# Kernel tuning notes

Hardware: AMD Instinct MI355X
Metric: run time of the kernel (lower is better)

## Reference

```python
import jax, jax.numpy as jnp
import numpy as np

K = 20

def lrelu(x):
    return jnp.where(x >= 0, x, 0.2 * x)

def get_graph_feature(x, k):
    # x: (B, N, C) channel-last. Returns (B, N, k, 2C) = [neighbor - x, x].
    inner = jnp.einsum('bnc,bmc->bnm', x, x)          # (B, N, N)
    sq = jnp.sum(x * x, axis=-1)                       # (B, N)
    # negative squared distance; top-k gives nearest neighbors (incl. self)
    neg_dist = 2.0 * inner - sq[:, :, None] - sq[:, None, :]
    _, idx = jax.lax.top_k(neg_dist, k)                # (B, N, k)
    neigh = jnp.take_along_axis(x[:, None, :, :], idx[:, :, :, None], axis=2)  # (B, N, k, C)
    center = jnp.broadcast_to(x[:, :, None, :], neigh.shape)
    return jnp.concatenate([neigh - center, center], axis=-1)

def setup_inputs() -> dict:
    key = jax.random.key(0)
    ks = jax.random.split(key, 12)
    B, N, input_dim = 32, 2048, 6
    emb_dim, out_dim = 1024, 40
    def w(k_, shape):
        fan_in = shape[-1]
        return jax.random.normal(k_, shape, dtype=jnp.float32) * (1.0 / np.sqrt(fan_in))
    return {
        'x':  jax.random.normal(ks[0], (B, N, input_dim), dtype=jnp.float32),
        'W1': w(ks[1], (64, 6)),            # conv1: 1x1 conv, no bias
        'W2': w(ks[2], (64, 128)),          # conv2
        'W5': w(ks[3], (emb_dim, 128)),     # conv5 (1d)
        'W3': w(ks[4], (32, input_dim - 3)),# conv3
        'W4': w(ks[5], (64, 32)),           # conv4
        'L1': w(ks[6], (128, (emb_dim + 64) * 2)),  # linear1, no bias
        'L2w': w(ks[7], (64, 128)),
        'L2b': jnp.zeros((64,), dtype=jnp.float32),
        'L3w': w(ks[8], (out_dim, 64)),
        'L3b': jnp.zeros((out_dim,), dtype=jnp.float32),
    }

def reference(x, W1, W2, W5, W3, W4, L1, L2w, L2b, L3w, L3b):
    x_pos = x[:, :, :3]       # (B, N, 3)
    x_feat = x[:, :, 3:]      # (B, N, input_dim-3)

    # EdgeConv block 1
    e = get_graph_feature(x_pos, K)                       # (B, N, k, 6)
    e = lrelu(jnp.einsum('bnkc,oc->bnko', e, W1))         # (B, N, k, 64)
    x1 = jnp.max(e, axis=2)                               # (B, N, 64)

    # EdgeConv block 2
    e = get_graph_feature(x1, K)                          # (B, N, k, 128)
    e = lrelu(jnp.einsum('bnkc,oc->bnko', e, W2))         # (B, N, k, 64)
    x2 = jnp.max(e, axis=2)                               # (B, N, 64)

    # conv5 over concatenated features
    h = jnp.concatenate([x1, x2], axis=-1)                # (B, N, 128)
    h = lrelu(jnp.einsum('bnc,oc->bno', h, W5))           # (B, N, emb)
    g = jnp.concatenate([jnp.max(h, axis=1), jnp.mean(h, axis=1)], axis=-1)  # (B, 2*emb)

    # per-point feature MLP (conv3 -> conv4)
    f = lrelu(jnp.einsum('bnc,oc->bno', x_feat, W3))      # (B, N, 32)
    f = lrelu(jnp.einsum('bnc,oc->bno', f, W4))           # (B, N, 64)
    fg = jnp.concatenate([jnp.max(f, axis=1), jnp.mean(f, axis=1)], axis=-1)  # (B, 128)

    z = jnp.concatenate([g, fg], axis=-1)                 # (B, (emb+64)*2)
    z = lrelu(z @ L1.T)
    z = lrelu(z @ L2w.T + L2b)
    return z @ L3w.T + L3b                                # (B, output)
```

## Files before the change

### kernel.cpp

```cpp
#include <hip/hip_runtime.h>
#include <math.h>

#define B_ 32
#define N_ 2048
#define KNN 20
#define FINF 3.402823466e38f
#define SCAP 256

typedef __attribute__((ext_vector_type(8))) short short8;
typedef __attribute__((ext_vector_type(4))) float f32x4;

#define OFF_X1   ((size_t)0)
#define OFF_X2   (OFF_X1 + (size_t)B_*N_*64*4)
#define OFF_SQ1  (OFF_X2 + (size_t)B_*N_*64*4)
#define OFF_IDX1 (OFF_SQ1 + (size_t)B_*N_*4)
#define OFF_IDX2 (OFF_IDX1 + (size_t)B_*N_*KNN*4)
#define OFF_PMAX (OFF_IDX2 + (size_t)B_*N_*KNN*4)
#define OFF_PSUM (OFF_PMAX + (size_t)B_*16*1024*4)
#define OFF_G    (OFF_PSUM + (size_t)B_*16*1024*4)
#define OFF_FG   (OFF_G + (size_t)B_*2048*4)
#define OFF_DIST (OFF_FG + (size_t)B_*128*4)
#define OFF_P    OFF_DIST
#define OFF_Q    (OFF_P + (size_t)B_*N_*64*4)
#define OFF_XHI  OFF_P
#define OFF_XLO  OFF_Q
#define OFF_WHI  (OFF_Q + (size_t)B_*N_*64*4)
#define OFF_WLO  (OFF_WHI + (size_t)1024*128*2)

__device__ __forceinline__ float lrelu(float x) { return x >= 0.0f ? x : 0.2f * x; }

template<class F>
__device__ __forceinline__ void wave_top20_slow(const float (&v)[32], int lane, int* out20, F idxf) {
    unsigned alive = 0xffffffffu;
    for (int sel = 0; sel < 20; ++sel) {
        float bv = -FINF;
        int bm = 0x7fffffff;
#pragma unroll
        for (int j = 0; j < 32; ++j) {
            bool a = (alive >> j) & 1u;
            bool better = a && (v[j] > bv);
            bv = better ? v[j] : bv;
            bm = better ? idxf(j) : bm;
        }
#pragma unroll
        for (int off = 32; off; off >>= 1) {
            float ov = __shfl_xor(bv, off, 64);
            int   om = __shfl_xor(bm, off, 64);
            bool take = (ov > bv) || (ov == bv && om < bm);
            bv = take ? ov : bv;
            bm = take ? om : bm;
        }
        if (lane == 0) out20[sel] = bm;
#pragma unroll
        for (int j = 0; j < 32; ++j)
            if (idxf(j) == bm) alive &= ~(1u << j);
    }
}

template<class F>
__device__ __forceinline__ void wave_top20_fast(const float (&v)[32], int lane,
                                                float* sval, int* sidx, int* out20, F idxf) {
    float lm = v[0];
#pragma unroll
    for (int j = 1; j < 32; ++j) lm = fmaxf(lm, v[j]);
    float s = lm;
#pragma unroll
    for (int k = 2; k <= 64; k <<= 1) {
#pragma unroll
        for (int j2 = k >> 1; j2 > 0; j2 >>= 1) {
            float o = __shfl_xor(s, j2, 64);
            bool up = ((lane & k) == 0);
            bool high = ((lane & j2) != 0);
            s = (high == up) ? fmaxf(s, o) : fminf(s, o);
        }
    }
    float that = __shfl(s, 44, 64);
    int cnt = 0;
    unsigned long long below = (lane == 63) ? 0xffffffffffffffffull >> 1
                                            : ((1ull << lane) - 1ull);
#pragma unroll
    for (int j = 0; j < 32; ++j) {
        bool p = (v[j] >= that);
        unsigned long long mk = __ballot(p);
        if (p) {
            int slot = cnt + (int)__popcll(mk & below);
            if (slot < SCAP) { sval[slot] = v[j]; sidx[slot] = idxf(j); }
        }
        cnt += (int)__popcll(mk);
    }
    int S = cnt;
    if (S > SCAP) {
        wave_top20_slow(v, lane, out20, idxf);
        return;
    }
    if (S <= 64) {
        bool ok = lane < S;
        float cv = ok ? sval[lane] : -FINF;
        int   cm = ok ? sidx[lane] : 0x7fffffff;
#pragma unroll
        for (int k = 2; k <= 64; k <<= 1) {
#pragma unroll
            for (int j2 = k >> 1; j2 > 0; j2 >>= 1) {
                float ov = __shfl_xor(cv, j2, 64);
                int   om = __shfl_xor(cm, j2, 64);
                bool up = ((lane & k) == 0);
                bool high = ((lane & j2) != 0);
                bool cur_first = (cv > ov) || (cv == ov && cm < om);
                bool take = (high == up) ? cur_first : !cur_first;
                cv = take ? ov : cv;
                cm = take ? om : cm;
            }
        }
        if (lane < 20) out20[lane] = cm;
    } else {
        float cv[4]; int cm[4]; unsigned alive = 0;
#pragma unroll
        for (int r = 0; r < 4; ++r) {
            int i = r * 64 + lane;
            bool ok = i < S;
            float vv = sval[i];
            int   mm = sidx[i];
            cv[r] = ok ? vv : -FINF;
            cm[r] = ok ? mm : 0x7fffffff;
            if (ok) alive |= 1u << r;
        }
        for (int sel = 0; sel < 20; ++sel) {
            float bv = -FINF; int bm = 0x7fffffff;
#pragma unroll
            for (int r = 0; r < 4; ++r) {
                bool a = (alive >> r) & 1u;
                bool better = a && (cv[r] > bv || (cv[r] == bv && cm[r] < bm));
                bv = better ? cv[r] : bv;
                bm = better ? cm[r] : bm;
            }
#pragma unroll
            for (int off = 32; off; off >>= 1) {
                float ov = __shfl_xor(bv, off, 64);
                int   om = __shfl_xor(bm, off, 64);
                bool take = (ov > bv) || (ov == bv && om < bm);
                bv = take ? ov : bv;
                bm = take ? om : bm;
            }
            if (lane == 0) out20[sel] = bm;
#pragma unroll
            for (int r = 0; r < 4; ++r)
                if (cm[r] == bm) alive &= ~(1u << r);
        }
    }
}

__global__ __launch_bounds__(256) void k1_knn_pos(const float* __restrict__ x,
                                                  int* __restrict__ idx1) {
    __shared__ float sP[N_ * 3];
    __shared__ float sval[4][SCAP];
    __shared__ int   sidx[4][SCAP];
    __shared__ int   sOut[4][20];
    int tid = threadIdx.x;
    int wid = tid >> 6, lane = tid & 63;
    int row = blockIdx.x * 4 + wid;
    int b = row >> 11, n = row & 2047;
    const float* xb = x + (size_t)b * N_ * 6;
    for (int m = tid; m < N_; m += 256) {
        float4 f = *(const float4*)(xb + m * 6);
        sP[m*3+0] = f.x; sP[m*3+1] = f.y; sP[m*3+2] = f.z;
    }
    __syncthreads();
    float cx = sP[n*3+0], cy = sP[n*3+1], cz = sP[n*3+2];
    float sqn = cx*cx + cy*cy + cz*cz;
    float v[32];
#pragma unroll
    for (int j = 0; j < 32; ++j) {
        int m = lane + (j << 6);
        float mx_ = sP[m*3+0], my = sP[m*3+1], mz = sP[m*3+2];
        float inner = cx*mx_ + cy*my + cz*mz;
        float sqm = mx_*mx_ + my*my + mz*mz;
        v[j] = 2.0f*inner - sqn - sqm;
    }
    wave_top20_fast(v, lane, sval[wid], sidx[wid], sOut[wid],
                    [lane](int j) { return lane + (j << 6); });
    __syncthreads();
    if (lane < 20) idx1[(size_t)row*KNN + lane] = sOut[wid][lane];
}

__global__ __launch_bounds__(256) void k2_conv1(const float* __restrict__ x,
                                                const int* __restrict__ idx1,
                                                const float* __restrict__ W1,
                                                float* __restrict__ x1,
                                                float* __restrict__ sq1) {
    int wid = threadIdx.x >> 6, o = threadIdx.x & 63;
    int row = blockIdx.x * 4 + wid;
    int b = row >> 11, n = row & 2047;
    const float* xb = x + (size_t)b * N_ * 6;
    float w0 = W1[o*6+0], w1 = W1[o*6+1], w2 = W1[o*6+2];
    float w3 = W1[o*6+3], w4 = W1[o*6+4], w5 = W1[o*6+5];
    float cx = xb[n*6+0], cy = xb[n*6+1], cz = xb[n*6+2];
    float base = w3*cx + w4*cy + w5*cz;
    float mx = -FINF;
    for (int k = 0; k < KNN; ++k) {
        int m = idx1[(size_t)row*KNN + k];
        float dx = xb[m*6+0]-cx, dy = xb[m*6+1]-cy, dz = xb[m*6+2]-cz;
        float s = base + w0*dx + w1*dy + w2*dz;
        s = lrelu(s);
        mx = fmaxf(mx, s);
    }
    x1[(size_t)row*64 + o] = mx;
    float sq = mx*mx;
#pragma unroll
    for (int off = 32; off; off >>= 1) sq += __shfl_xor(sq, off, 64);
    if (o == 0) sq1[row] = sq;
}

__global__ __launch_bounds__(256) void k3_dist(const float* __restrict__ x1,
                                               const float* __restrict__ sq1,
                                               float* __restrict__ dist, int b0) {
    __shared__ float sA[32][128];
    __shared__ float sB[32][128];
    int t = blockIdx.x;
    int I = (int)((sqrtf(8.0f*t + 1.0f) - 1.0f) * 0.5f);
    while ((I+1)*(I+2)/2 <= t) ++I;
    while (I*(I+1)/2 > t) --I;
    int J = t - I*(I+1)/2;
    int b = b0 + blockIdx.y;
    const float* Xb  = x1  + (size_t)b * N_ * 64;
    const float* sqb = sq1 + (size_t)b * N_;
    float* Db = dist + (size_t)blockIdx.y * N_ * N_;
    int i0 = I*128, j0 = J*128;
    int tid = threadIdx.x;
    float acc[8][8] = {};
    for (int kt = 0; kt < 64; kt += 32) {
#pragma unroll
        for (int l = 0; l < 4; ++l) {
            int v = l*256 + tid;
            int i = v >> 3, cg = (v & 7) << 2;
            float4 fa = *(const float4*)(Xb + (size_t)(i0+i)*64 + kt + cg);
            sA[cg+0][i] = fa.x; sA[cg+1][i] = fa.y; sA[cg+2][i] = fa.z; sA[cg+3][i] = fa.w;
            float4 fb = *(const float4*)(Xb + (size_t)(j0+i)*64 + kt + cg);
            sB[cg+0][i] = fb.x; sB[cg+1][i] = fb.y; sB[cg+2][i] = fb.z; sB[cg+3][i] = fb.w;
        }
        __syncthreads();
        int ti = (tid & 15) * 8, tj = (tid >> 4) * 8;
#pragma unroll 4
        for (int c = 0; c < 32; ++c) {
            float a[8], w[8];
            *(float4*)&a[0] = *(const float4*)&sA[c][ti];
            *(float4*)&a[4] = *(const float4*)&sA[c][ti+4];
            *(float4*)&w[0] = *(const float4*)&sB[c][tj];
            *(float4*)&w[4] = *(const float4*)&sB[c][tj+4];
#pragma unroll
            for (int ii = 0; ii < 8; ++ii)
#pragma unroll
                for (int jj = 0; jj < 8; ++jj)
                    acc[ii][jj] = fmaf(a[ii], w[jj], acc[ii][jj]);
        }
        __syncthreads();
    }
    int ti = (tid & 15) * 8, tj = (tid >> 4) * 8;
    float sqi[8], sqj[8];
#pragma unroll
    for (int ii = 0; ii < 8; ++ii) sqi[ii] = sqb[i0 + ti + ii];
#pragma unroll
    for (int jj = 0; jj < 8; ++jj) sqj[jj] = sqb[j0 + tj + jj];
#pragma unroll
    for (int ii = 0; ii < 8; ++ii) {
        float ov[8];
#pragma unroll
        for (int jj = 0; jj < 8; ++jj) ov[jj] = 2.0f*acc[ii][jj] - sqi[ii] - sqj[jj];
        float4* p = (float4*)(Db + (size_t)(i0+ti+ii)*N_ + j0 + tj);
        p[0] = *(float4*)&ov[0]; p[1] = *(float4*)&ov[4];
    }
    if (I != J) {
#pragma unroll
        for (int jj = 0; jj < 8; ++jj) {
            float ov[8];
#pragma unroll
            for (int ii = 0; ii < 8; ++ii) ov[ii] = 2.0f*acc[ii][jj] - sqi[ii] - sqj[jj];
            float4* p = (float4*)(Db + (size_t)(j0+tj+jj)*N_ + i0 + ti);
            p[0] = *(float4*)&ov[0]; p[1] = *(float4*)&ov[4];
        }
    }
}

__global__ __launch_bounds__(256) void k4_topk(const float* __restrict__ dist,
                                               int* __restrict__ idx2, int b0) {
    __shared__ float sval[4][SCAP];
    __shared__ int   sidx[4][SCAP];
    __shared__ int   sOut[4][20];
    int wid = threadIdx.x >> 6, lane = threadIdx.x & 63;
    int lrow = blockIdx.x * 4 + wid;
    int lb = lrow >> 11, n = lrow & 2047;
    const float4* Dr4 = (const float4*)(dist + (size_t)lb * N_ * N_ + (size_t)n * N_);
    float v[32];
#pragma unroll
    for (int j4 = 0; j4 < 8; ++j4) {
        float4 f = Dr4[(j4 << 6) + lane];
        v[j4*4+0] = f.x; v[j4*4+1] = f.y; v[j4*4+2] = f.z; v[j4*4+3] = f.w;
    }
    wave_top20_fast(v, lane, sval[wid], sidx[wid], sOut[wid],
                    [lane](int j) { return (lane << 2) + ((j >> 2) << 8) + (j & 3); });
    __syncthreads();
    int row = (b0 + lb) * N_ + n;
    if (lane < 20) idx2[(size_t)row*KNN + lane] = sOut[wid][lane];
}

__global__ __launch_bounds__(256) void k5pre_pq(const float* __restrict__ x1,
                                                const float* __restrict__ W2,
                                                float* __restrict__ P,
                                                float* __restrict__ Q) {
    int w = threadIdx.x >> 6, o = threadIdx.x & 63;
    float wd[64], wc[64];
    const float* wsrc = W2 + (size_t)o * 128;
#pragma unroll
    for (int j = 0; j < 16; ++j) {
        float4 d = *(const float4*)(wsrc + j*4);
        float4 c = *(const float4*)(wsrc + 64 + j*4);
        wd[j*4+0] = d.x; wd[j*4+1] = d.y; wd[j*4+2] = d.z; wd[j*4+3] = d.w;
        wc[j*4+0] = c.x - d.x; wc[j*4+1] = c.y - d.y; wc[j*4+2] = c.z - d.z; wc[j*4+3] = c.w - d.w;
    }
    int row0 = (blockIdx.x * 4 + w) * 32;
    for (int r = 0; r < 32; ++r) {
        const float* xr = x1 + (size_t)(row0 + r) * 64;
        float p = 0.0f, q = 0.0f;
#pragma unroll
        for (int j = 0; j < 16; ++j) {
            float4 xc = *(const float4*)(xr + j*4);
            p = fmaf(wd[j*4+0], xc.x, p); q = fmaf(wc[j*4+0], xc.x, q);
            p = fmaf(wd[j*4+1], xc.y, p); q = fmaf(wc[j*4+1], xc.y, q);
            p = fmaf(wd[j*4+2], xc.z, p); q = fmaf(wc[j*4+2], xc.z, q);
            p = fmaf(wd[j*4+3], xc.w, p); q = fmaf(wc[j*4+3], xc.w, q);
        }
        P[(size_t)(row0 + r) * 64 + o] = p;
        Q[(size_t)(row0 + r) * 64 + o] = q;
    }
}

__global__ __launch_bounds__(256) void k5b_max(const float* __restrict__ P,
                                               const float* __restrict__ Q,
                                               const int* __restrict__ idx2,
                                               float* __restrict__ x2) {
    int w = threadIdx.x >> 6, lane = threadIdx.x & 63;
    int row = blockIdx.x * 4 + w;
    int b = row >> 11;
    float q = Q[(size_t)row * 64 + lane];
    const int* id = idx2 + (size_t)row * KNN;
    const float* Pb = P + ((size_t)b << 11) * 64;
    int midx[KNN];
#pragma unroll
    for (int k = 0; k < KNN; ++k) midx[k] = id[k];
    float mx = -FINF;
#pragma unroll
    for (int k = 0; k < KNN; ++k) {
        float p = Pb[(size_t)midx[k] * 64 + lane];
        mx = fmaxf(mx, lrelu(p + q));
    }
    x2[(size_t)row * 64 + lane] = mx;
}

__global__ __launch_bounds__(256) void k6pre_split(const float* __restrict__ x1,
                                                   const float* __restrict__ x2,
                                                   const float* __restrict__ W5,
                                                   unsigned short* __restrict__ Xhi,
                                                   unsigned short* __restrict__ Xlo,
                                                   unsigned short* __restrict__ Whi,
                                                   unsigned short* __restrict__ Wlo) {
    const int NX = B_ * N_ * 128 / 4;
    int e4 = blockIdx.x * 256 + threadIdx.x;
    float4 v;
    unsigned short* dh; unsigned short* dl; size_t doff;
    if (e4 < NX) {
        int r = e4 >> 5, c4 = (e4 & 31) << 2;
        v = (c4 < 64) ? *(const float4*)(x1 + (size_t)r*64 + c4)
                      : *(const float4*)(x2 + (size_t)r*64 + (c4 - 64));
        dh = Xhi; dl = Xlo; doff = (size_t)r*128 + c4;
    } else {
        int e = e4 - NX;
        if (e >= 1024*128/4) return;
        int r = e >> 5, c4 = (e & 31) << 2;
        v = *(const float4*)(W5 + (size_t)r*128 + c4);
        dh = Whi; dl = Wlo; doff = (size_t)r*128 + c4;
    }
    float a[4] = {v.x, v.y, v.z, v.w};
    unsigned short hh[4], ll[4];
#pragma unroll
    for (int i = 0; i < 4; ++i) {
        unsigned u = __float_as_uint(a[i]);
        unsigned r16 = (u + 0x7fffu + ((u >> 16) & 1u)) >> 16;
        hh[i] = (unsigned short)r16;
        float lo = a[i] - __uint_as_float(r16 << 16);
        unsigned ul = __float_as_uint(lo);
        ll[i] = (unsigned short)((ul + 0x7fffu + ((ul >> 16) & 1u)) >> 16);
    }
    *(uint2*)(dh + doff) = make_uint2((unsigned)hh[0] | ((unsigned)hh[1] << 16),
                                      (unsigned)hh[2] | ((unsigned)hh[3] << 16));
    *(uint2*)(dl + doff) = make_uint2((unsigned)ll[0] | ((unsigned)ll[1] << 16),
                                      (unsigned)ll[2] | ((unsigned)ll[3] << 16));
}

__global__ __launch_bounds__(256) void k6a_mfma(const unsigned short* __restrict__ Xhi,
                                                const unsigned short* __restrict__ Xlo,
                                                const unsigned short* __restrict__ Whi,
                                                const unsigned short* __restrict__ Wlo,
                                                float* __restrict__ pmax,
                                                float* __restrict__ psum) {
    __shared__ unsigned short sT[4][128*32];
    __shared__ float redmx[128][2], redsm[128][2];
    int tid = threadIdx.x;
    int nt = blockIdx.x >> 3, ot = blockIdx.x & 7, b = blockIdx.y;
    int wid = tid >> 6, lane = tid & 63;
    int wn = wid & 1, wo = wid >> 1;
    int sub = lane & 15, quad = lane >> 4;
    const unsigned short* gp[4];
    gp[0] = Xhi + (size_t)(b*2048 + nt*128) * 128;
    gp[1] = Xlo + (size_t)(b*2048 + nt*128) * 128;
    gp[2] = Whi + (size_t)(ot*128) * 128;
    gp[3] = Wlo + (size_t)(ot*128) * 128;
    f32x4 acc[4][4];
#pragma unroll
    for (int i = 0; i < 4; ++i)
#pragma unroll
        for (int j = 0; j < 4; ++j) acc[i][j] = (f32x4)0.0f;
    for (int kt = 0; kt < 4; ++kt) {
        int k0 = kt * 32;
        __syncthreads();
#pragma unroll
        for (int it = 0; it < 8; ++it) {
            int task = it*256 + tid;
            int tile = task >> 9, rem = task & 511;
            int row = rem >> 2, ch = rem & 3;
            uint4 d = *(const uint4*)(gp[tile] + (size_t)row*128 + k0 + ch*8);
            *(uint4*)(&sT[tile][row*32 + ch*8]) = d;
        }
        __syncthreads();
        short8 ah[4], al[4], bh[4], bl[4];
#pragma unroll
        for (int mi = 0; mi < 4; ++mi) {
            int r = wn*64 + mi*16 + sub;
            ah[mi] = *(const short8*)(&sT[0][r*32 + quad*8]);
            al[mi] = *(const short8*)(&sT[1][r*32 + quad*8]);
        }
#pragma unroll
        for (int ni = 0; ni < 4; ++ni) {
            int r = wo*64 + ni*16 + sub;
            bh[ni] = *(const short8*)(&sT[2][r*32 + quad*8]);
            bl[ni] = *(const short8*)(&sT[3][r*32 + quad*8]);
        }
#pragma unroll
        for (int mi = 0; mi < 4; ++mi)
#pragma unroll
            for (int ni = 0; ni < 4; ++ni) {
                acc[mi][ni] = __builtin_amdgcn_mfma_f32_16x16x32_bf16(ah[mi], bh[ni], acc[mi][ni], 0, 0, 0);
                acc[mi][ni] = __builtin_amdgcn_mfma_f32_16x16x32_bf16(ah[mi], bl[ni], acc[mi][ni], 0, 0, 0);
                acc[mi][ni] = __builtin_amdgcn_mfma_f32_16x16x32_bf16(al[mi], bh[ni], acc[mi][ni], 0, 0, 0);
            }
    }
#pragma unroll
    for (int ni = 0; ni < 4; ++ni) {
        float mx = -FINF, sm = 0.0f;
#pragma unroll
        for (int mi = 0; mi < 4; ++mi)
#pragma unroll
            for (int r = 0; r < 4; ++r) {
                float v = lrelu(acc[mi][ni][r]);
                mx = fmaxf(mx, v); sm += v;
            }
        mx = fmaxf(mx, __shfl_xor(mx, 16, 64));
        mx = fmaxf(mx, __shfl_xor(mx, 32, 64));
        sm += __shfl_xor(sm, 16, 64);
        sm += __shfl_xor(sm, 32, 64);
        if (quad == 0) {
            redmx[wo*64 + ni*16 + sub][wn] = mx;
            redsm[wo*64 + ni*16 + sub][wn] = sm;
        }
    }
    __syncthreads();
    if (tid < 128) {
        float mx = fmaxf(redmx[tid][0], redmx[tid][1]);
        float sm = redsm[tid][0] + redsm[tid][1];
        size_t po = ((size_t)b*16 + nt)*1024 + ot*128 + tid;
        pmax[po] = mx; psum[po] = sm;
    }
}

__global__ __launch_bounds__(256) void k6b_reduce(const float* __restrict__ pmax,
                                                  const float* __restrict__ psum,
                                                  float* __restrict__ g) {
    int t = blockIdx.x * 256 + threadIdx.x;
    int b = t >> 10, o = t & 1023;
    float mx = -FINF, sm = 0.0f;
    for (int i = 0; i < 16; ++i) {
        mx = fmaxf(mx, pmax[((size_t)b*16 + i)*1024 + o]);
        sm += psum[((size_t)b*16 + i)*1024 + o];
    }
    g[(size_t)b*2048 + o] = mx;
    g[(size_t)b*2048 + 1024 + o] = sm * (1.0f/2048.0f);
}

__global__ __launch_bounds__(256) void k7_feat(const float* __restrict__ x,
                                               const float* __restrict__ W3,
                                               const float* __restrict__ W4,
                                               float* __restrict__ fg) {
    __shared__ float rmx[16*256];
    __shared__ float rsm[16*256];
    int b = blockIdx.y, og = blockIdx.x;
    int o0 = og * 16;
    int tid = threadIdx.x;
    float mx[16], sm[16];
#pragma unroll
    for (int i = 0; i < 16; ++i) { mx[i] = -FINF; sm[i] = 0.0f; }
    for (int n = tid; n < N_; n += 256) {
        const float* xr = x + ((size_t)b*N_ + n)*6 + 3;
        float f0 = xr[0], f1 = xr[1], f2 = xr[2];
        float h1[32];
#pragma unroll
        for (int j = 0; j < 32; ++j) {
            float s = W3[j*3]*f0 + W3[j*3+1]*f1 + W3[j*3+2]*f2;
            h1[j] = lrelu(s);
        }
#pragma unroll
        for (int oi = 0; oi < 16; ++oi) {
            float s = 0.0f;
#pragma unroll
            for (int j = 0; j < 32; ++j) s = fmaf(W4[(o0+oi)*32 + j], h1[j], s);
            s = lrelu(s);
            mx[oi] = fmaxf(mx[oi], s); sm[oi] += s;
        }
    }
#pragma unroll
    for (int oi = 0; oi < 16; ++oi) { rmx[oi*256 + tid] = mx[oi]; rsm[oi*256 + tid] = sm[oi]; }
    __syncthreads();
    for (int s = 128; s > 0; s >>= 1) {
        if (tid < s) {
#pragma unroll
            for (int oi = 0; oi < 16; ++oi) {
                rmx[oi*256 + tid] = fmaxf(rmx[oi*256 + tid], rmx[oi*256 + tid + s]);
                rsm[oi*256 + tid] += rsm[oi*256 + tid + s];
            }
        }
        __syncthreads();
    }
    if (tid < 16) {
        fg[(size_t)b*128 + o0 + tid]      = rmx[tid*256];
        fg[(size_t)b*128 + 64 + o0 + tid] = rsm[tid*256] * (1.0f/2048.0f);
    }
}

__global__ __launch_bounds__(128) void k8_head(const float* __restrict__ g,
                                               const float* __restrict__ fg,
                                               const float* __restrict__ L1w,
                                               const float* __restrict__ L2w,
                                               const float* __restrict__ L2b,
                                               const float* __restrict__ L3w,
                                               const float* __restrict__ L3b,
                                               float* __restrict__ out) {
    __shared__ float sz[2176];
    __shared__ float s1[128];
    __shared__ float s2[64];
    int b = blockIdx.x, tid = threadIdx.x;
    for (int c = tid; c < 2048; c += 128) sz[c] = g[(size_t)b*2048 + c];
    if (tid < 128) sz[2048 + tid] = fg[(size_t)b*128 + tid];
    __syncthreads();
    {
        float a = 0.0f;
        const float* w = L1w + (size_t)tid * 2176;
        for (int c = 0; c < 2176; ++c) a = fmaf(w[c], sz[c], a);
        s1[tid] = lrelu(a);
    }
    __syncthreads();
    if (tid < 64) {
        float a = L2b[tid];
        for (int c = 0; c < 128; ++c) a = fmaf(L2w[tid*128 + c], s1[c], a);
        s2[tid] = lrelu(a);
    }
    __syncthreads();
    if (tid < 40) {
        float a = L3b[tid];
        for (int c = 0; c < 64; ++c) a = fmaf(L3w[tid*64 + c], s2[c], a);
        out[(size_t)b*40 + tid] = a;
    }
}

extern "C" void kernel_launch(void* const* d_in, const int* in_sizes, int n_in,
                              void* d_out, int out_size, void* d_ws, size_t ws_size,
                              hipStream_t stream) {
    const float* x   = (const float*)d_in[0];
    const float* W1  = (const float*)d_in[1];
    const float* W2  = (const float*)d_in[2];
    const float* W5  = (const float*)d_in[3];
    const float* W3  = (const float*)d_in[4];
    const float* W4  = (const float*)d_in[5];
    const float* L1w = (const float*)d_in[6];
    const float* L2w = (const float*)d_in[7];
    const float* L2b = (const float*)d_in[8];
    const float* L3w = (const float*)d_in[9];
    const float* L3b = (const float*)d_in[10];
    float* out = (float*)d_out;

    char* ws = (char*)d_ws;
    float* x1   = (float*)(ws + OFF_X1);
    float* x2   = (float*)(ws + OFF_X2);
    float* sq1  = (float*)(ws + OFF_SQ1);
    int*   idx1 = (int*)  (ws + OFF_IDX1);
    int*   idx2 = (int*)  (ws + OFF_IDX2);
    float* pmax = (float*)(ws + OFF_PMAX);
    float* psum = (float*)(ws + OFF_PSUM);
    float* g    = (float*)(ws + OFF_G);
    float* fg   = (float*)(ws + OFF_FG);
    float* dist = (float*)(ws + OFF_DIST);
    float* P    = (float*)(ws + OFF_P);
    float* Q    = (float*)(ws + OFF_Q);
    unsigned short* Xhi = (unsigned short*)(ws + OFF_XHI);
    unsigned short* Xlo = (unsigned short*)(ws + OFF_XLO);
    unsigned short* Whi = (unsigned short*)(ws + OFF_WHI);
    unsigned short* Wlo = (unsigned short*)(ws + OFF_WLO);

    size_t distBytes = (size_t)N_ * N_ * 4;
    size_t availB = (ws_size > OFF_DIST) ? (ws_size - OFF_DIST) : 0;
    int maxcb = (int)(availB / distBytes);
    int cb = 4;
    while (cb * 2 <= maxcb && cb * 2 <= 32) cb <<= 1;

    k1_knn_pos<<<16384, 256, 0, stream>>>(x, idx1);
    k2_conv1<<<16384, 256, 0, stream>>>(x, idx1, W1, x1, sq1);
    for (int b0 = 0; b0 < 32; b0 += cb) {
        k3_dist<<<dim3(136, cb), 256, 0, stream>>>(x1, sq1, dist, b0);
        k4_topk<<<cb * 512, 256, 0, stream>>>(dist, idx2, b0);
    }
    k5pre_pq<<<512, 256, 0, stream>>>(x1, W2, P, Q);
    k5b_max<<<16384, 256, 0, stream>>>(P, Q, idx2, x2);
    k6pre_split<<<8320, 256, 0, stream>>>(x1, x2, W5, Xhi, Xlo, Whi, Wlo);
    k6a_mfma<<<dim3(128, 32), 256, 0, stream>>>(Xhi, Xlo, Whi, Wlo, pmax, psum);
    k6b_reduce<<<128, 256, 0, stream>>>(pmax, psum, g);
    k7_feat<<<dim3(4, 32), 256, 0, stream>>>(x, W3, W4, fg);
    k8_head<<<32, 128, 0, stream>>>(g, fg, L1w, L2w, L2b, L3w, L3b, out);
}
```

Measured before the change: 863.7 us.

## Fuse bf16 split into k5b, process two rows per wave in kNN, drop sOut staging

The bf16 hi/lo split of x1/x2 is folded into the k5b_max kernel, so x2 is no longer re-read by a separate split pass, and only W5 is split in a small kernel. k1_knn_pos now handles two query rows per wave with float4-padded shared positions, halving the grid and sharing neighbor loads. Top-k results are written straight to global memory instead of going through shared memory and a block barrier, and SCAP shrinks from 256 to 192 to cut LDS use. The workspace layout moves Xhi/Xlo after P/Q and places W splits in the idx1 region, which relies on idx1 being dead by then. Fewer candidates can be kept before falling back to the slow selection path, and the per-element 16-bit stores in k5b are less coalesced than the old vector stores.

```diff
diff --git a/kernel.cpp b/kernel.cpp
--- a/kernel.cpp
+++ b/kernel.cpp
@@ -5,7 +5,7 @@
 #define N_ 2048
 #define KNN 20
 #define FINF 3.402823466e38f
-#define SCAP 256
+#define SCAP 192
 
 typedef __attribute__((ext_vector_type(8))) short short8;
 typedef __attribute__((ext_vector_type(4))) float f32x4;
@@ -21,16 +21,25 @@
 #define OFF_FG   (OFF_G + (size_t)B_*2048*4)
 #define OFF_DIST (OFF_FG + (size_t)B_*128*4)
 #define OFF_P    OFF_DIST
-#define OFF_Q    (OFF_P + (size_t)B_*N_*64*4)
-#define OFF_XHI  OFF_P
-#define OFF_XLO  OFF_Q
-#define OFF_WHI  (OFF_Q + (size_t)B_*N_*64*4)
+#define OFF_Q    (OFF_P   + (size_t)B_*N_*64*4)
+#define OFF_XHI  (OFF_Q   + (size_t)B_*N_*64*4)
+#define OFF_XLO  (OFF_XHI + (size_t)B_*N_*128*2)
+#define OFF_WHI  OFF_IDX1
 #define OFF_WLO  (OFF_WHI + (size_t)1024*128*2)
 
 __device__ __forceinline__ float lrelu(float x) { return x >= 0.0f ? x : 0.2f * x; }
 
+__device__ __forceinline__ void bf16split(float a, unsigned short& hi, unsigned short& lo) {
+    unsigned u = __float_as_uint(a);
+    unsigned r16 = (u + 0x7fffu + ((u >> 16) & 1u)) >> 16;
+    hi = (unsigned short)r16;
+    float l = a - __uint_as_float(r16 << 16);
+    unsigned ul = __float_as_uint(l);
+    lo = (unsigned short)((ul + 0x7fffu + ((ul >> 16) & 1u)) >> 16);
+}
+
 template<class F>
-__device__ __forceinline__ void wave_top20_slow(const float (&v)[32], int lane, int* out20, F idxf) {
+__device__ __forceinline__ void wave_top20_slow(const float (&v)[32], int lane, int* gout, F idxf) {
     unsigned alive = 0xffffffffu;
     for (int sel = 0; sel < 20; ++sel) {
         float bv = -FINF;
@@ -50,7 +59,7 @@
             bv = take ? ov : bv;
             bm = take ? om : bm;
         }
-        if (lane == 0) out20[sel] = bm;
+        if (lane == 0) gout[sel] = bm;
 #pragma unroll
         for (int j = 0; j < 32; ++j)
             if (idxf(j) == bm) alive &= ~(1u << j);
@@ -59,7 +68,7 @@
 
 template<class F>
 __device__ __forceinline__ void wave_top20_fast(const float (&v)[32], int lane,
-                                                float* sval, int* sidx, int* out20, F idxf) {
+                                                float* sval, int* sidx, int* gout, F idxf) {
     float lm = v[0];
 #pragma unroll
     for (int j = 1; j < 32; ++j) lm = fmaxf(lm, v[j]);
@@ -90,7 +99,7 @@
     }
     int S = cnt;
     if (S > SCAP) {
-        wave_top20_slow(v, lane, out20, idxf);
+        wave_top20_slow(v, lane, gout, idxf);
         return;
     }
     if (S <= 64) {
@@ -111,11 +120,11 @@
                 cm = take ? om : cm;
             }
         }
-        if (lane < 20) out20[lane] = cm;
+        if (lane < 20) gout[lane] = cm;
     } else {
-        float cv[4]; int cm[4]; unsigned alive = 0;
-#pragma unroll
-        for (int r = 0; r < 4; ++r) {
+        float cv[3]; int cm[3]; unsigned alive = 0;
+#pragma unroll
+        for (int r = 0; r < 3; ++r) {
             int i = r * 64 + lane;
             bool ok = i < S;
             float vv = sval[i];
@@ -127,7 +136,7 @@
         for (int sel = 0; sel < 20; ++sel) {
             float bv = -FINF; int bm = 0x7fffffff;
 #pragma unroll
-            for (int r = 0; r < 4; ++r) {
+            for (int r = 0; r < 3; ++r) {
                 bool a = (alive >> r) & 1u;
                 bool better = a && (cv[r] > bv || (cv[r] == bv && cm[r] < bm));
                 bv = better ? cv[r] : bv;
@@ -141,9 +150,9 @@
                 bv = take ? ov : bv;
                 bm = take ? om : bm;
             }
-            if (lane == 0) out20[sel] = bm;
-#pragma unroll
-            for (int r = 0; r < 4; ++r)
+            if (lane == 0) gout[sel] = bm;
+#pragma unroll
+            for (int r = 0; r < 3; ++r)
                 if (cm[r] == bm) alive &= ~(1u << r);
         }
     }
@@ -151,35 +160,37 @@
 
 __global__ __launch_bounds__(256) void k1_knn_pos(const float* __restrict__ x,
                                                   int* __restrict__ idx1) {
-    __shared__ float sP[N_ * 3];
+    __shared__ float4 sP4[N_];
     __shared__ float sval[4][SCAP];
     __shared__ int   sidx[4][SCAP];
-    __shared__ int   sOut[4][20];
     int tid = threadIdx.x;
     int wid = tid >> 6, lane = tid & 63;
-    int row = blockIdx.x * 4 + wid;
-    int b = row >> 11, n = row & 2047;
+    int row0 = blockIdx.x * 8 + wid * 2;
+    int b = row0 >> 11, n0 = row0 & 2047;
     const float* xb = x + (size_t)b * N_ * 6;
     for (int m = tid; m < N_; m += 256) {
         float4 f = *(const float4*)(xb + m * 6);
-        sP[m*3+0] = f.x; sP[m*3+1] = f.y; sP[m*3+2] = f.z;
+        f.w = 0.0f;
+        sP4[m] = f;
     }
     __syncthreads();
-    float cx = sP[n*3+0], cy = sP[n*3+1], cz = sP[n*3+2];
-    float sqn = cx*cx + cy*cy + cz*cz;
-    float v[32];
+    float4 c0 = sP4[n0], c1 = sP4[n0 + 1];
+    float sq0 = c0.x*c0.x + c0.y*c0.y + c0.z*c0.z;
+    float sq1v = c1.x*c1.x + c1.y*c1.y + c1.z*c1.z;
+    float v0[32], v1[32];
 #pragma unroll
     for (int j = 0; j < 32; ++j) {
         int m = lane + (j << 6);
-        float mx_ = sP[m*3+0], my = sP[m*3+1], mz = sP[m*3+2];
-        float inner = cx*mx_ + cy*my + cz*mz;
-        float sqm = mx_*mx_ + my*my + mz*mz;
-        v[j] = 2.0f*inner - sqn - sqm;
-    }
-    wave_top20_fast(v, lane, sval[wid], sidx[wid], sOut[wid],
-                    [lane](int j) { return lane + (j << 6); });
-    __syncthreads();
-    if (lane < 20) idx1[(size_t)row*KNN + lane] = sOut[wid][lane];
+        float4 p = sP4[m];
+        float sqm = p.x*p.x + p.y*p.y + p.z*p.z;
+        float d0 = c0.x*p.x + c0.y*p.y + c0.z*p.z;
+        float d1 = c1.x*p.x + c1.y*p.y + c1.z*p.z;
+        v0[j] = 2.0f*d0 - sq0 - sqm;
+        v1[j] = 2.0f*d1 - sq1v - sqm;
+    }
+    auto idxf = [lane](int j) { return lane + (j << 6); };
+    wave_top20_fast(v0, lane, sval[wid], sidx[wid], idx1 + (size_t)row0 * KNN, idxf);
+    wave_top20_fast(v1, lane, sval[wid], sidx[wid], idx1 + (size_t)(row0 + 1) * KNN, idxf);
 }
 
 __global__ __launch_bounds__(256) void k2_conv1(const float* __restrict__ x,
@@ -284,7 +295,6 @@
                                                int* __restrict__ idx2, int b0) {
     __shared__ float sval[4][SCAP];
     __shared__ int   sidx[4][SCAP];
-    __shared__ int   sOut[4][20];
     int wid = threadIdx.x >> 6, lane = threadIdx.x & 63;
     int lrow = blockIdx.x * 4 + wid;
     int lb = lrow >> 11, n = lrow & 2047;
@@ -295,11 +305,9 @@
         float4 f = Dr4[(j4 << 6) + lane];
         v[j4*4+0] = f.x; v[j4*4+1] = f.y; v[j4*4+2] = f.z; v[j4*4+3] = f.w;
     }
-    wave_top20_fast(v, lane, sval[wid], sidx[wid], sOut[wid],
+    int row = (b0 + lb) * N_ + n;
+    wave_top20_fast(v, lane, sval[wid], sidx[wid], idx2 + (size_t)row * KNN,
                     [lane](int j) { return (lane << 2) + ((j >> 2) << 8) + (j & 3); });
-    __syncthreads();
-    int row = (b0 + lb) * N_ + n;
-    if (lane < 20) idx2[(size_t)row*KNN + lane] = sOut[wid][lane];
 }
 
 __global__ __launch_bounds__(256) void k5pre_pq(const float* __restrict__ x1,
@@ -336,7 +344,10 @@
 __global__ __launch_bounds__(256) void k5b_max(const float* __restrict__ P,
                                                const float* __restrict__ Q,
                                                const int* __restrict__ idx2,
-                                               float* __restrict__ x2) {
+                                               const float* __restrict__ x1,
+                                               float* __restrict__ x2,
+                                               unsigned short* __restrict__ Xhi,
+                                               unsigned short* __restrict__ Xlo) {
     int w = threadIdx.x >> 6, lane = threadIdx.x & 63;
     int row = blockIdx.x * 4 + w;
     int b = row >> 11;
@@ -353,46 +364,30 @@
         mx = fmaxf(mx, lrelu(p + q));
     }
     x2[(size_t)row * 64 + lane] = mx;
-}
-
-__global__ __launch_bounds__(256) void k6pre_split(const float* __restrict__ x1,
-                                                   const float* __restrict__ x2,
-                                                   const float* __restrict__ W5,
-                                                   unsigned short* __restrict__ Xhi,
-                                                   unsigned short* __restrict__ Xlo,
-                                                   unsigned short* __restrict__ Whi,
-                                                   unsigned short* __restrict__ Wlo) {
-    const int NX = B_ * N_ * 128 / 4;
-    int e4 = blockIdx.x * 256 + threadIdx.x;
-    float4 v;
-    unsigned short* dh; unsigned short* dl; size_t doff;
-    if (e4 < NX) {
-        int r = e4 >> 5, c4 = (e4 & 31) << 2;
-        v = (c4 < 64) ? *(const float4*)(x1 + (size_t)r*64 + c4)
-                      : *(const float4*)(x2 + (size_t)r*64 + (c4 - 64));
-        dh = Xhi; dl = Xlo; doff = (size_t)r*128 + c4;
-    } else {
-        int e = e4 - NX;
-        if (e >= 1024*128/4) return;
-        int r = e >> 5, c4 = (e & 31) << 2;
-        v = *(const float4*)(W5 + (size_t)r*128 + c4);
-        dh = Whi; dl = Wlo; doff = (size_t)r*128 + c4;
-    }
+    float x1v = x1[(size_t)row * 64 + lane];
+    unsigned short h0, l0, h1, l1;
+    bf16split(x1v, h0, l0);
+    bf16split(mx,  h1, l1);
+    size_t base = (size_t)row * 128 + lane;
+    Xhi[base] = h0;      Xlo[base] = l0;
+    Xhi[base + 64] = h1; Xlo[base + 64] = l1;
+}
+
+__global__ __launch_bounds__(256) void k6pre_wsplit(const float* __restrict__ W5,
+                                                    unsigned short* __restrict__ Whi,
+                                                    unsigned short* __restrict__ Wlo) {
+    int e = blockIdx.x * 256 + threadIdx.x;
+    int r = e >> 5, c4 = (e & 31) << 2;
+    float4 v = *(const float4*)(W5 + (size_t)r*128 + c4);
     float a[4] = {v.x, v.y, v.z, v.w};
     unsigned short hh[4], ll[4];
 #pragma unroll
-    for (int i = 0; i < 4; ++i) {
-        unsigned u = __float_as_uint(a[i]);
-        unsigned r16 = (u + 0x7fffu + ((u >> 16) & 1u)) >> 16;
-        hh[i] = (unsigned short)r16;
-        float lo = a[i] - __uint_as_float(r16 << 16);
-        unsigned ul = __float_as_uint(lo);
-        ll[i] = (unsigned short)((ul + 0x7fffu + ((ul >> 16) & 1u)) >> 16);
-    }
-    *(uint2*)(dh + doff) = make_uint2((unsigned)hh[0] | ((unsigned)hh[1] << 16),
-                                      (unsigned)hh[2] | ((unsigned)hh[3] << 16));
-    *(uint2*)(dl + doff) = make_uint2((unsigned)ll[0] | ((unsigned)ll[1] << 16),
-                                      (unsigned)ll[2] | ((unsigned)ll[3] << 16));
+    for (int i = 0; i < 4; ++i) bf16split(a[i], hh[i], ll[i]);
+    size_t doff = (size_t)r*128 + c4;
+    *(uint2*)(Whi + doff) = make_uint2((unsigned)hh[0] | ((unsigned)hh[1] << 16),
+                                       (unsigned)hh[2] | ((unsigned)hh[3] << 16));
+    *(uint2*)(Wlo + doff) = make_uint2((unsigned)ll[0] | ((unsigned)ll[1] << 16),
+                                       (unsigned)ll[2] | ((unsigned)ll[3] << 16));
 }
 
 __global__ __launch_bounds__(256) void k6a_mfma(const unsigned short* __restrict__ Xhi,
@@ -618,15 +613,15 @@
     int cb = 4;
     while (cb * 2 <= maxcb && cb * 2 <= 32) cb <<= 1;
 
-    k1_knn_pos<<<16384, 256, 0, stream>>>(x, idx1);
+    k1_knn_pos<<<8192, 256, 0, stream>>>(x, idx1);
     k2_conv1<<<16384, 256, 0, stream>>>(x, idx1, W1, x1, sq1);
     for (int b0 = 0; b0 < 32; b0 += cb) {
         k3_dist<<<dim3(136, cb), 256, 0, stream>>>(x1, sq1, dist, b0);
         k4_topk<<<cb * 512, 256, 0, stream>>>(dist, idx2, b0);
     }
     k5pre_pq<<<512, 256, 0, stream>>>(x1, W2, P, Q);
-    k5b_max<<<16384, 256, 0, stream>>>(P, Q, idx2, x2);
-    k6pre_split<<<8320, 256, 0, stream>>>(x1, x2, W5, Xhi, Xlo, Whi, Wlo);
+    k5b_max<<<16384, 256, 0, stream>>>(P, Q, idx2, x1, x2, Xhi, Xlo);
+    k6pre_wsplit<<<128, 256, 0, stream>>>(W5, Whi, Wlo);
     k6a_mfma<<<dim3(128, 32), 256, 0, stream>>>(Xhi, Xlo, Whi, Wlo, pmax, psum);
     k6b_reduce<<<128, 256, 0, stream>>>(pmax, psum, g);
     k7_feat<<<dim3(4, 32), 256, 0, stream>>>(x, W3, W4, fg);
```

New measurement: 918.3 us. 6.3% more time.
